# Kernel tuning notes

Hardware: AMD Instinct MI355X
Metric: run time of the kernel (lower is better)

The kernel has to match this reference:

```python
import jax, jax.numpy as jnp
import numpy as np

G = 4  # groupsize((1,1)) = 4 -> C4 rotations, exact rot90 path


def _lift_filter(w):
    # w: (O, I, k, k) -> (O*G, I, k, k); orbit of 90-degree filter rotations
    f = jnp.stack([jnp.rot90(w, r, axes=(-2, -1)) for r in range(G)], axis=1)
    O, _, I, k, _ = f.shape
    return f.reshape(O * G, I, k, k)


def _group_filter(w):
    # w: (O, I, G, k, k) -> (O*G, I*G, k, k)
    # rotatestack_n: spatial rot90 by r, then cyclic shift of the group axis by r
    fs = []
    for r in range(G):
        roty = jnp.rot90(w, r, axes=(-2, -1))
        roty = jnp.roll(roty, r, axis=-3)  # new[i] = roty[(G - r + i) % G]
        fs.append(roty)
    f = jnp.stack(fs, axis=1)  # (O, G, I, G, k, k)
    O, _, I, _, k, _ = f.shape
    return f.reshape(O * G, I * G, k, k)


def _conv(x, f, b, pad):
    y = jax.lax.conv_general_dilated(x, f, (1, 1), [(pad, pad), (pad, pad)],
                                     dimension_numbers=('NCHW', 'OIHW', 'NCHW'))
    # bias is stacked per group element: repeat each out-channel bias G times
    return y + jnp.repeat(b, G)[None, :, None, None]


def _pool(x):
    return jax.lax.reduce_window(x, -jnp.inf, jax.lax.max, (1, 1, 2, 2), (1, 1, 2, 2), 'VALID')


def setup_inputs():
    key = jax.random.key(0)
    ks = jax.random.split(key, 16)
    ch = [6, 12, 12, 24, 24, 16]   # [24,48,48,96,96,64] // G
    kern = [7, 5, 5, 5, 5, 5]
    d = {'x': jax.random.normal(ks[0], (64, 1, 96, 96), jnp.float32)}
    d['w0'] = jax.random.normal(ks[1], (ch[0], 1, kern[0], kern[0]), jnp.float32) / np.sqrt(ch[0] * 1.0)
    d['b0'] = jnp.zeros((ch[0],), jnp.float32)
    for i in range(1, 6):
        std = 1.0 / np.sqrt(float(ch[i] * ch[i - 1]))
        d['w%d' % i] = jax.random.normal(ks[1 + i], (ch[i], ch[i - 1], G, kern[i], kern[i]), jnp.float32) * std
        d['b%d' % i] = jnp.zeros((ch[i],), jnp.float32)
    d['fw1'] = jax.random.normal(ks[8], (64, 64), jnp.float32) * 0.05
    d['fb1'] = jnp.zeros((64,), jnp.float32)
    d['fw2'] = jax.random.normal(ks[9], (10, 64), jnp.float32) * 0.05
    d['fb2'] = jnp.zeros((10,), jnp.float32)
    return d


def reference(x, w0, b0, w1, b1, w2, b2, w3, b3, w4, b4, w5, b5, fw1, fb1, fw2, fb2):
    h = jax.nn.relu(_conv(x, _lift_filter(w0), b0, 1))                  # (B,24,92,92)
    h = jax.nn.relu(_conv(h, _group_filter(w1), b1, 2))
    h = _pool(h)                                                        # (B,48,46,46)
    h = jax.nn.relu(_conv(h, _group_filter(w2), b2, 2))
    h = jax.nn.relu(_conv(h, _group_filter(w3), b3, 2))
    h = _pool(h)                                                        # (B,96,23,23)
    h = jax.nn.relu(_conv(h, _group_filter(w4), b4, 2))
    h = jax.nn.relu(_conv(h, _group_filter(w5), b5, 1))                 # (B,64,21,21)
    h = h.mean(axis=(-2, -1))                                           # (B,64) flat (out_ch*G)
    h = jax.nn.relu(h @ fw1.T + fb1)
    return h @ fw2.T + fb2                                              # (B,10)
```

## Files before the change

### kernel.cpp

```cpp
#include <hip/hip_runtime.h>
#include <hip/hip_bf16.h>


typedef short s16x8 __attribute__((ext_vector_type(8)));
typedef __bf16 bf16x8 __attribute__((ext_vector_type(8)));
typedef float f32x4 __attribute__((ext_vector_type(4)));
typedef unsigned short u16;
typedef unsigned int u32;

__device__ __forceinline__ u16 f2bf(float f) {
    unsigned u = __float_as_uint(f);
    return (u16)((u + 0x7FFFu + ((u >> 16) & 1u)) >> 16);
}
__device__ __forceinline__ float bf2f(u16 h) {
    return __uint_as_float(((unsigned)h) << 16);
}

__device__ __forceinline__ void rot_src(int r, int K, int y, int x, int& sy, int& sx) {
    switch (r & 3) {
        case 0: sy = y;         sx = x;         break;
        case 1: sy = x;         sx = K - 1 - y; break;
        case 2: sy = K - 1 - y; sx = K - 1 - x; break;
        default: sy = K - 1 - x; sx = y;        break;
    }
}

__global__ void lift_w0T_kernel(const float* __restrict__ w, float* __restrict__ f) {
    const int K = 7, KK = 49, OC = 24;
    int idx = blockIdx.x * blockDim.x + threadIdx.x;
    if (idx >= KK * OC) return;
    int oc = idx % OC; int kk = idx / OC;
    int y = kk / K, x = kk % K;
    int r = oc & 3, o = oc >> 2;
    int sy, sx; rot_src(r, K, y, x, sy, sx);
    f[idx] = w[o * KK + sy * K + sx];
}

__global__ void wfrag_kernel(const float* __restrict__ w, u16* __restrict__ wf,
                             int O, int I, int KC, int NT, int total) {
    int idx = blockIdx.x * blockDim.x + threadIdx.x;
    if (idx >= total) return;
    int j = idx & 7;
    int lane = (idx >> 3) & 63;
    int rest = idx >> 9;
    int nc = rest % NT; rest /= NT;
    int kc = rest % KC; int kpos = rest / KC;
    int ky = kpos / 5, kx = kpos % 5;
    int kk = ((lane >> 4) << 3) + j;
    int ic = kc * 32 + kk;
    int oc = nc * 16 + (lane & 15);
    float val = 0.f;
    if (ic < I * 4) {
        int o = oc >> 2, r = oc & 3, i = ic >> 2, s = ic & 3;
        int g = (s - r + 4) & 3;
        int sy, sx; rot_src(r, 5, ky, kx, sy, sx);
        val = w[(((o * I + i) * 4 + g) * 25) + sy * 5 + sx];
    }
    u16 hb = f2bf(val);
    u16 lb = f2bf(val - bf2f(hb));
    wf[idx] = hb;
    wf[idx + total] = lb;
}

__global__ void pad_x_kernel(const float* __restrict__ x, float* __restrict__ xp) {
    int idx = blockIdx.x * blockDim.x + threadIdx.x;
    if (idx >= 64 * 96 * 96) return;
    int c = idx % 96; int t = idx / 96;
    int r = t % 96; int n = t / 96;
    xp[((size_t)n * 98 + r + 1) * 100 + c + 1] = x[idx];
}

__global__ void prep_halo_kernel(u16* __restrict__ buf, long LO, int NHW,
                                 int Hp, int Wp, int ICO) {
    int idx = blockIdx.x * blockDim.x + threadIdx.x;
    if (idx >= NHW) return;
    int c = idx % Wp; int t = idx / Wp;
    int r = t % Hp; int n = t / Hp;
    bool halo = (r < 2) || (r >= Hp - 2) || (c < 2) || (c >= Wp - 2);
    if (!halo) return;
    size_t base = (((size_t)n * Hp + r) * Wp + c) * ICO;
    s16x8 z = {0, 0, 0, 0, 0, 0, 0, 0};
    for (int cc = 0; cc < (ICO >> 3); ++cc) {
        *(s16x8*)(buf + base + cc * 8) = z;
        *(s16x8*)(buf + LO + base + cc * 8) = z;
    }
}

__global__ __launch_bounds__(256) void conv0_kernel(
        const float* __restrict__ xp, const float* __restrict__ f0t,
        const float* __restrict__ b0, u16* __restrict__ p1, long p1LO) {
    int idx = blockIdx.x * blockDim.x + threadIdx.x;
    if (idx >= 64 * 92 * 23) return;
    int xq = idx % 23; int t = idx / 23;
    int oy = t % 92; int n = t / 92;
    float acc[24][4];
#pragma unroll
    for (int a = 0; a < 24; ++a)
#pragma unroll
        for (int b = 0; b < 4; ++b) acc[a][b] = 0.f;

    const float* ip = xp + ((size_t)n * 98 + oy) * 100 + xq * 4;
#pragma unroll
    for (int ky = 0; ky < 7; ++ky) {
        const float* row = ip + (size_t)ky * 100;
        float xv[12];
#pragma unroll
        for (int v = 0; v < 3; ++v)
            *reinterpret_cast<float4*>(&xv[4 * v]) =
                *reinterpret_cast<const float4*>(row + 4 * v);
#pragma unroll
        for (int kx = 0; kx < 7; ++kx) {
            const float* wp = f0t + (ky * 7 + kx) * 24;
#pragma unroll
            for (int qd = 0; qd < 6; ++qd) {
                float4 wv = *reinterpret_cast<const float4*>(wp + qd * 4);
#pragma unroll
                for (int jx = 0; jx < 4; ++jx) {
                    acc[qd * 4 + 0][jx] = fmaf(wv.x, xv[kx + jx], acc[qd * 4 + 0][jx]);
                    acc[qd * 4 + 1][jx] = fmaf(wv.y, xv[kx + jx], acc[qd * 4 + 1][jx]);
                    acc[qd * 4 + 2][jx] = fmaf(wv.z, xv[kx + jx], acc[qd * 4 + 2][jx]);
                    acc[qd * 4 + 3][jx] = fmaf(wv.w, xv[kx + jx], acc[qd * 4 + 3][jx]);
                }
            }
        }
    }
    float bv[6];
#pragma unroll
    for (int qd = 0; qd < 6; ++qd) bv[qd] = b0[qd];

    size_t ob = (((size_t)n * 96 + oy + 2) * 96 + xq * 4 + 2) * 24;
#pragma unroll
    for (int jx = 0; jx < 4; ++jx) {
        s16x8 hv[3], lv[3];
#pragma unroll
        for (int cc = 0; cc < 3; ++cc)
#pragma unroll
            for (int e = 0; e < 8; ++e) {
                int ch = cc * 8 + e;
                float v = fmaxf(acc[ch][jx] + bv[ch >> 2], 0.f);
                u16 hb = f2bf(v);
                u16 lb = f2bf(v - bf2f(hb));
                hv[cc][e] = (short)hb; lv[cc][e] = (short)lb;
            }
#pragma unroll
        for (int cc = 0; cc < 3; ++cc) {
            *(s16x8*)(p1 + ob + jx * 24 + cc * 8) = hv[cc];
            *(s16x8*)(p1 + p1LO + ob + jx * 24 + cc * 8) = lv[cc];
        }
    }
}

template <int IC32, int ICIN, int NT, int NTW, int MT, int CR, int SW, bool POOL,
          int XOFF, int OCO, bool TRANS, int PMODE>
__global__ __launch_bounds__(SW*(NT/NTW)*64, 2) void conv_mfma_kernel(
        const u16* __restrict__ act, long actLO,
        const u16* __restrict__ wf, int wfLO,
        const float* __restrict__ bias,
        u16* __restrict__ outP, long outLO,
        float* __restrict__ outF,
        int Hp, int Wp, int OH, int OW, int PH, int POW,
        int NRG, int NXS, int HpO, int WpO) {
    constexpr int OG = NT / NTW;
    constexpr int NW = SW * OG;
    constexpr int KC = IC32 / 32;
    constexpr int WT = MT * 16 + 4 + XOFF;
    constexpr int R  = CR * SW + 4;
    constexpr int CHUNKS = R * WT * 8;
    constexpr int TROWS = POOL ? SW : CR * SW;
    constexpr int TX = POOL ? MT * 8 : MT * 16;
    constexpr int SX = OCO + 4;
    constexpr int STAGE_B = CHUNKS * 16;
    constexpr int TRAN_B = TRANS ? TROWS * TX * SX * 4 : 0;
    constexpr int LDSB = STAGE_B > TRAN_B ? STAGE_B : TRAN_B;
    __shared__ __align__(16) char ldsraw[LDSB];
    u16* lds = (u16*)ldsraw;

    int q8 = gridDim.x >> 3;
    int wid = (blockIdx.x & 7) * q8 + (blockIdx.x >> 3);
    int xs = wid % NXS; int t0 = wid / NXS;
    int rgrp = t0 % NRG; int n = t0 / NRG;

    int BR = rgrp * (CR * SW);
    int rbase = BR + XOFF;
    int xbase = xs * (MT * 16);

    int tid = threadIdx.x;
    int wv = tid >> 6;
    int lane = tid & 63;
    int l15 = lane & 15, lg = lane >> 4;
    int og = wv % OG, rg = wv / OG;

    f32x4 accP[CR][MT][NTW], accQ[CR][MT][NTW];
#pragma unroll
    for (int cr = 0; cr < CR; ++cr)
#pragma unroll
        for (int m = 0; m < MT; ++m)
#pragma unroll
            for (int nc = 0; nc < NTW; ++nc) {
                accP[cr][m][nc] = f32x4{0.f, 0.f, 0.f, 0.f};
                accQ[cr][m][nc] = f32x4{0.f, 0.f, 0.f, 0.f};
            }

    const u16* wfl = wf + (size_t)lane * 8;
    const u16* actn = act + ((size_t)n * Hp) * Wp * ICIN;

    for (int kcp = 0; kcp < KC; ++kcp) {
        if (kcp) __syncthreads();
        for (int u = tid; u < CHUNKS; u += NW * 64) {
            int c = u & 7; int rest = u >> 3;
            int xl = rest % WT; int row = rest / WT;
            int cg = c ^ (xl & 7);
            int sp = cg >> 2, cc4 = cg & 3;
            int gx = xbase + xl, gr = rbase + row;
            int ch0 = (kcp * 4 + cc4) * 8;
            s16x8 v = {0, 0, 0, 0, 0, 0, 0, 0};
            if (gx < Wp && gr < Hp && ch0 < ICIN)
                v = *(const s16x8*)(actn + (size_t)sp * actLO +
                      ((size_t)gr * Wp + gx) * ICIN + ch0);
            *(s16x8*)&lds[(size_t)u * 8] = v;
        }
        __syncthreads();

        auto loadB = [&](int w, bf16x8 (&bh)[NTW], bf16x8 (&bl)[NTW]) {
            const u16* bp = wfl + ((size_t)(w * KC + kcp) * NT + og * NTW) * 512;
#pragma unroll
            for (int nc = 0; nc < NTW; ++nc) {
                bh[nc] = *(const bf16x8*)(bp + nc * 512);
                bl[nc] = *(const bf16x8*)(bp + nc * 512 + wfLO);
            }
        };

        if constexpr (PMODE == 1) {
            auto loadA = [&](int w, bf16x8 (&ah)[MT][CR], bf16x8 (&al)[MT][CR]) {
                int wky = w / 5, wkx = w - wky * 5;
#pragma unroll
                for (int m = 0; m < MT; ++m) {
                    int xl = m * 16 + XOFF + l15 + wkx;
                    int sw = xl & 7;
#pragma unroll
                    for (int cr = 0; cr < CR; ++cr) {
                        int row = rg * CR + cr + wky;
                        int base = (row * WT + xl) * 8;
                        ah[m][cr] = *(const bf16x8*)&lds[(size_t)(base + (lg ^ sw)) * 8];
                        al[m][cr] = *(const bf16x8*)&lds[(size_t)(base + ((4 + lg) ^ sw)) * 8];
                    }
                }
            };
            auto mfmaBlk = [&](bf16x8 (&bh)[NTW], bf16x8 (&bl)[NTW],
                               bf16x8 (&ah)[MT][CR], bf16x8 (&al)[MT][CR]) {
#pragma unroll
                for (int m = 0; m < MT; ++m)
#pragma unroll
                    for (int nc = 0; nc < NTW; ++nc)
#pragma unroll
                        for (int cr = 0; cr < CR; ++cr) {
                            accP[cr][m][nc] = __builtin_amdgcn_mfma_f32_16x16x32_bf16(
                                ah[m][cr], bh[nc], accP[cr][m][nc], 0, 0, 0);
                            accQ[cr][m][nc] = __builtin_amdgcn_mfma_f32_16x16x32_bf16(
                                ah[m][cr], bl[nc], accQ[cr][m][nc], 0, 0, 0);
                            accQ[cr][m][nc] = __builtin_amdgcn_mfma_f32_16x16x32_bf16(
                                al[m][cr], bh[nc], accQ[cr][m][nc], 0, 0, 0);
                        }
            };
            bf16x8 bhX[NTW], blX[NTW], ahX[MT][CR], alX[MT][CR];
            bf16x8 bhY[NTW], blY[NTW], ahY[MT][CR], alY[MT][CR];
            loadB(0, bhX, blX); loadA(0, ahX, alX);
            for (int t = 0; t < 12; ++t) {
                loadB(2 * t + 1, bhY, blY); loadA(2 * t + 1, ahY, alY);
                mfmaBlk(bhX, blX, ahX, alX);
                loadB(2 * t + 2, bhX, blX); loadA(2 * t + 2, ahX, alX);
                mfmaBlk(bhY, blY, ahY, alY);
            }
            mfmaBlk(bhX, blX, ahX, alX);
        } else {
            auto window = [&](int w, bf16x8 (&bh)[NTW], bf16x8 (&bl)[NTW]) {
                int wky = w / 5, wkx = w - wky * 5;
#pragma unroll
                for (int m = 0; m < MT; ++m) {
                    int xl = m * 16 + XOFF + l15 + wkx;
                    int sw = xl & 7;
                    bf16x8 ah[CR], al[CR];
#pragma unroll
                    for (int cr = 0; cr < CR; ++cr) {
                        int row = rg * CR + cr + wky;
                        int base = (row * WT + xl) * 8;
                        ah[cr] = *(const bf16x8*)&lds[(size_t)(base + (lg ^ sw)) * 8];
                        al[cr] = *(const bf16x8*)&lds[(size_t)(base + ((4 + lg) ^ sw)) * 8];
                    }
#pragma unroll
                    for (int nc = 0; nc < NTW; ++nc)
#pragma unroll
                        for (int cr = 0; cr < CR; ++cr) {
                            accP[cr][m][nc] = __builtin_amdgcn_mfma_f32_16x16x32_bf16(
                                ah[cr], bh[nc], accP[cr][m][nc], 0, 0, 0);
                            accQ[cr][m][nc] = __builtin_amdgcn_mfma_f32_16x16x32_bf16(
                                ah[cr], bl[nc], accQ[cr][m][nc], 0, 0, 0);
                            accQ[cr][m][nc] = __builtin_amdgcn_mfma_f32_16x16x32_bf16(
                                al[cr], bh[nc], accQ[cr][m][nc], 0, 0, 0);
                        }
                }
            };
            bf16x8 bhX[NTW], blX[NTW], bhY[NTW], blY[NTW];
            loadB(0, bhX, blX);
            for (int t = 0; t < 12; ++t) {
                loadB(2 * t + 1, bhY, blY);
                window(2 * t, bhX, blX);
                loadB(2 * t + 2, bhX, blX);
                window(2 * t + 1, bhY, blY);
            }
            window(24, bhX, blX);
        }
    }

    if constexpr (TRANS) {
        __syncthreads();
        u32* ldsw = (u32*)ldsraw;
#pragma unroll
        for (int nc = 0; nc < NTW; ++nc) {
            int oc = (og * NTW + nc) * 16 + l15;
            float bv = bias[oc >> 2];
#pragma unroll
            for (int m = 0; m < MT; ++m) {
                if constexpr (POOL) {
                    float c0[4], c1[4];
#pragma unroll
                    for (int j = 0; j < 4; ++j) {
                        c0[j] = accP[0][m][nc][j] + accQ[0][m][nc][j];
                        c1[j] = accP[1][m][nc][j] + accQ[1][m][nc][j];
                    }
#pragma unroll
                    for (int a2 = 0; a2 < 2; ++a2) {
                        float mx = fmaxf(fmaxf(c0[2 * a2], c0[2 * a2 + 1]),
                                         fmaxf(c1[2 * a2], c1[2 * a2 + 1]));
                        float v = fmaxf(mx + bv, 0.f);
                        u16 hb = f2bf(v);
                        u16 lb = f2bf(v - bf2f(hb));
                        int px = m * 8 + lg * 2 + a2;
                        ldsw[(rg * TX + px) * SX + oc] = ((u32)hb << 16) | lb;
                    }
                } else {
#pragma unroll
                    for (int cr = 0; cr < CR; ++cr)
#pragma unroll
                        for (int j = 0; j < 4; ++j) {
                            float v = fmaxf(accP[cr][m][nc][j] + accQ[cr][m][nc][j] + bv, 0.f);
                            u16 hb = f2bf(v);
                            u16 lb = f2bf(v - bf2f(hb));
                            int xloc = m * 16 + lg * 4 + j;
                            ldsw[((rg * CR + cr) * TX + xloc) * SX + oc] =
                                ((u32)hb << 16) | lb;
                        }
                }
            }
        }
        __syncthreads();
        constexpr int CPX = OCO / 8;
        constexpr int TOT = TROWS * TX * 2 * CPX;
        int OHL = POOL ? PH : OH;
        int OWL = POOL ? POW : OW;
        int obr = POOL ? rgrp * SW : BR;
        int obx = POOL ? (xbase >> 1) : xbase;
        for (int u = tid; u < TOT; u += NW * 64) {
            int c = u % CPX; int rest = u / CPX;
            int pl = rest & 1; rest >>= 1;
            int x = rest % TX; int row = rest / TX;
            int gr = obr + row, gx = obx + x;
            if (gr >= OHL || gx >= OWL) continue;
            s16x8 v = {0, 0, 0, 0, 0, 0, 0, 0};
            if (c * 8 < NT * 16) {
                const u32* p = &ldsw[(row * TX + x) * SX + c * 8];
                uint4 w0 = *(const uint4*)p;
                uint4 w1 = *(const uint4*)(p + 4);
                if (pl == 0) {
                    v[0] = (short)(w0.x >> 16); v[1] = (short)(w0.y >> 16);
                    v[2] = (short)(w0.z >> 16); v[3] = (short)(w0.w >> 16);
                    v[4] = (short)(w1.x >> 16); v[5] = (short)(w1.y >> 16);
                    v[6] = (short)(w1.z >> 16); v[7] = (short)(w1.w >> 16);
                } else {
                    v[0] = (short)(w0.x & 0xffff); v[1] = (short)(w0.y & 0xffff);
                    v[2] = (short)(w0.z & 0xffff); v[3] = (short)(w0.w & 0xffff);
                    v[4] = (short)(w1.x & 0xffff); v[5] = (short)(w1.y & 0xffff);
                    v[6] = (short)(w1.z & 0xffff); v[7] = (short)(w1.w & 0xffff);
                }
            }
            *(s16x8*)(outP + (size_t)pl * outLO +
                      (((size_t)n * HpO + gr + 2) * WpO + gx + 2) * OCO + c * 8) = v;
        }
    } else {
#pragma unroll
        for (int nc = 0; nc < NTW; ++nc) {
            int oc = (og * NTW + nc) * 16 + l15;
            float bv = bias[oc >> 2];
#pragma unroll
            for (int m = 0; m < MT; ++m) {
                int gx0 = xbase + m * 16;
#pragma unroll
                for (int cr = 0; cr < CR; ++cr) {
                    int oy = BR + rg * CR + cr;
                    if (oy < OH) {
#pragma unroll
                        for (int j = 0; j < 4; ++j) {
                            int gx = gx0 + lg * 4 + j;
                            if (gx < OW) {
                                float v = fmaxf(accP[cr][m][nc][j] + accQ[cr][m][nc][j] + bv, 0.f);
                                outF[(((size_t)n * OH + oy) * OW + gx) * (NT * 16) + oc] = v;
                            }
                        }
                    }
                }
            }
        }
    }
}

__global__ void mean_nhwc_kernel(const float* __restrict__ in, float* __restrict__ out) {
    __shared__ float sm[256];
    int n = blockIdx.x;
    int c = threadIdx.x & 63, q = threadIdx.x >> 6;
    float s = 0.f;
    for (int p = q; p < 441; p += 4) s += in[((size_t)n * 441 + p) * 64 + c];
    sm[threadIdx.x] = s;
    __syncthreads();
    if (q == 0) out[n * 64 + c] = (sm[c] + sm[c + 64] + sm[c + 128] + sm[c + 192]) * (1.0f / 441.0f);
}

__global__ void fc_kernel(const float* __restrict__ mean, const float* __restrict__ fw1,
                          const float* __restrict__ fb1, const float* __restrict__ fw2,
                          const float* __restrict__ fb2, float* __restrict__ out) {
    __shared__ float m[4096];
    __shared__ float h1[4096];
    int tid = threadIdx.x;
    for (int i = tid; i < 4096; i += 256) m[i] = mean[i];
    __syncthreads();
    for (int i = tid; i < 4096; i += 256) {
        int n = i >> 6, j = i & 63;
        float s = fb1[j];
        for (int k = 0; k < 64; ++k) s = fmaf(m[n * 64 + k], fw1[j * 64 + k], s);
        h1[i] = fmaxf(s, 0.f);
    }
    __syncthreads();
    for (int i = tid; i < 640; i += 256) {
        int n = i / 10, j2 = i % 10;
        float s = fb2[j2];
        for (int j = 0; j < 64; ++j) s = fmaf(h1[n * 64 + j], fw2[j2 * 64 + j], s);
        out[i] = s;
    }
}

extern "C" void kernel_launch(void* const* d_in, const int* in_sizes, int n_in,
                              void* d_out, int out_size, void* d_ws, size_t ws_size,
                              hipStream_t stream) {
    const float* x   = (const float*)d_in[0];
    const float* w0  = (const float*)d_in[1];
    const float* b0  = (const float*)d_in[2];
    const float* w1  = (const float*)d_in[3];
    const float* b1  = (const float*)d_in[4];
    const float* w2  = (const float*)d_in[5];
    const float* b2  = (const float*)d_in[6];
    const float* w3  = (const float*)d_in[7];
    const float* b3  = (const float*)d_in[8];
    const float* w4  = (const float*)d_in[9];
    const float* b4  = (const float*)d_in[10];
    const float* w5  = (const float*)d_in[11];
    const float* b5  = (const float*)d_in[12];
    const float* fw1 = (const float*)d_in[13];
    const float* fb1 = (const float*)d_in[14];
    const float* fw2 = (const float*)d_in[15];
    const float* fb2 = (const float*)d_in[16];

    char* ws = (char*)d_ws;
    if (ws_size < 128827392ull) return;

    float* F0   = (float*)(ws + 0);
    u16*   WF1  = (u16*)(ws + 8192);
    u16*   WF2  = (u16*)(ws + 161792);
    u16*   WF3  = (u16*)(ws + 468992);
    u16*   WF4  = (u16*)(ws + 1083392);
    u16*   WF5  = (u16*)(ws + 2004992);
    float* MEANB= (float*)(ws + 2619392);
    float* XP   = (float*)(ws + 2635776);
    float* C5   = (float*)(ws + 5144576);
    u16*   A    = (u16*)(ws + 12369920);
    u16*   B    = (u16*)(ws + 87867392);
    const long P1LO = 14155776;
    const long P2LO = 10240000;
    const long P4LO = 4478976;

    hipLaunchKernelGGL(lift_w0T_kernel, dim3(5), dim3(256), 0, stream, w0, F0);
    hipLaunchKernelGGL(wfrag_kernel, dim3(150), dim3(256), 0, stream, w1, WF1, 12, 6, 1, 3, 38400);
    hipLaunchKernelGGL(wfrag_kernel, dim3(300), dim3(256), 0, stream, w2, WF2, 12, 12, 2, 3, 76800);
    hipLaunchKernelGGL(wfrag_kernel, dim3(600), dim3(256), 0, stream, w3, WF3, 24, 12, 2, 6, 153600);
    hipLaunchKernelGGL(wfrag_kernel, dim3(900), dim3(256), 0, stream, w4, WF4, 24, 24, 3, 6, 230400);
    hipLaunchKernelGGL(wfrag_kernel, dim3(600), dim3(256), 0, stream, w5, WF5, 16, 24, 3, 4, 153600);

    hipMemsetAsync(XP, 0, 2508800, stream);
    hipLaunchKernelGGL(pad_x_kernel, dim3(2304), dim3(256), 0, stream, x, XP);

    hipLaunchKernelGGL(prep_halo_kernel, dim3(2304), dim3(256), 0, stream,
                       A, P1LO, 64*96*96, 96, 96, 24);
    hipLaunchKernelGGL(conv0_kernel, dim3((64*92*23 + 255)/256), dim3(256), 0, stream,
                       XP, F0, b0, A, P1LO);

    hipLaunchKernelGGL(prep_halo_kernel, dim3(625), dim3(256), 0, stream,
                       B, P2LO, 64*50*50, 50, 50, 64);
    hipLaunchKernelGGL((conv_mfma_kernel<32, 24, 3, 3, 3, 2, 4, true, 0, 64, true, 0>),
                       dim3(1536), dim3(256), 0, stream,
                       A, P1LO, WF1, 38400, b1, B, P2LO, (float*)nullptr,
                       96, 96, 92, 92, 46, 46, 12, 2, 50, 50);

    hipLaunchKernelGGL(prep_halo_kernel, dim3(625), dim3(256), 0, stream,
                       A, P2LO, 64*50*50, 50, 50, 64);
    hipLaunchKernelGGL((conv_mfma_kernel<64, 64, 3, 3, 3, 1, 4, false, 0, 64, true, 1>),
                       dim3(768), dim3(256), 0, stream,
                       B, P2LO, WF2, 76800, b2, A, P2LO, (float*)nullptr,
                       50, 50, 46, 46, 0, 0, 12, 1, 50, 50);

    hipLaunchKernelGGL(prep_halo_kernel, dim3(183), dim3(256), 0, stream,
                       B, P4LO, 64*27*27, 27, 27, 96);
    hipLaunchKernelGGL((conv_mfma_kernel<64, 64, 6, 3, 3, 2, 2, true, 0, 96, true, 0>),
                       dim3(768), dim3(256), 0, stream,
                       A, P2LO, WF3, 153600, b3, B, P4LO, (float*)nullptr,
                       50, 50, 46, 46, 23, 23, 12, 1, 27, 27);

    hipLaunchKernelGGL(prep_halo_kernel, dim3(183), dim3(256), 0, stream,
                       A, P4LO, 64*27*27, 27, 27, 96);
    hipLaunchKernelGGL((conv_mfma_kernel<96, 96, 6, 3, 2, 2, 2, false, 0, 96, true, 1>),
                       dim3(384), dim3(256), 0, stream,
                       B, P4LO, WF4, 230400, b4, A, P4LO, (float*)nullptr,
                       27, 27, 23, 23, 0, 0, 6, 1, 27, 27);

    hipLaunchKernelGGL((conv_mfma_kernel<96, 96, 4, 2, 2, 2, 2, false, 1, 96, false, 1>),
                       dim3(384), dim3(256), 0, stream,
                       A, P4LO, WF5, 153600, b5, (u16*)A, 0, C5,
                       27, 27, 21, 21, 0, 0, 6, 1, 27, 27);

    hipLaunchKernelGGL(mean_nhwc_kernel, dim3(64), dim3(256), 0, stream, C5, MEANB);
    hipLaunchKernelGGL(fc_kernel, dim3(1), dim3(256), 0, stream,
                       MEANB, fw1, fb1, fw2, fb2, (float*)d_out);
}
```

Measured before the change: 571.8 us.

## Fold kx taps into K dimension for layer-1 conv to cut padded MFMA work

Layer 1 has only 24 input channels, so the old kernel padded each 32-wide K chunk per tap and wasted a quarter of the MFMA work. The new conv_fold_kernel packs (kx, channel-octet) pairs into K chunks of 32, giving 20 steps instead of 25. A new weight-fragment kernel lays weights out to match. The step loop is fully unrolled with double-buffered B loads, which adds register pressure and irregular LDS indexing per lane group.

```diff
diff --git a/kernel.cpp b/kernel.cpp
--- a/kernel.cpp
+++ b/kernel.cpp
@@ -62,6 +62,34 @@
     wf[idx + total] = lb;
 }
 
+__global__ void wfrag_fold_kernel(const float* __restrict__ w, u16* __restrict__ wf,
+                                  int O, int I, int PASSES, int NT, int ICR8,
+                                  int total) {
+    int idx = blockIdx.x * blockDim.x + threadIdx.x;
+    if (idx >= total) return;
+    int j = idx & 7;
+    int lane = (idx >> 3) & 63;
+    int rest = idx >> 9;
+    int nc = rest % NT; rest /= NT;
+    int p = rest % PASSES; int ky = rest / PASSES;
+    int kchunk = p * 4 + (lane >> 4);
+    float val = 0.f;
+    if (kchunk < 5 * ICR8) {
+        int kx = kchunk / ICR8;
+        int icc = kchunk - kx * ICR8;
+        int ic = icc * 8 + j;
+        int oc = nc * 16 + (lane & 15);
+        int o = oc >> 2, r = oc & 3, i = ic >> 2, s = ic & 3;
+        int g = (s - r + 4) & 3;
+        int sy, sx; rot_src(r, 5, ky, kx, sy, sx);
+        val = w[(((o * I + i) * 4 + g) * 25) + sy * 5 + sx];
+    }
+    u16 hb = f2bf(val);
+    u16 lb = f2bf(val - bf2f(hb));
+    wf[idx] = hb;
+    wf[idx + total] = lb;
+}
+
 __global__ void pad_x_kernel(const float* __restrict__ x, float* __restrict__ xp) {
     int idx = blockIdx.x * blockDim.x + threadIdx.x;
     if (idx >= 64 * 96 * 96) return;
@@ -150,9 +178,9 @@
     }
 }
 
-template <int IC32, int ICIN, int NT, int NTW, int MT, int CR, int SW, bool POOL,
-          int XOFF, int OCO, bool TRANS, int PMODE>
-__global__ __launch_bounds__(SW*(NT/NTW)*64, 2) void conv_mfma_kernel(
+template <int ICR8, int ICIN, int PASSES, int NT, int NTW, int MT, int CR, int SW,
+          bool POOL, int XOFF, int OCO, bool TRANS>
+__global__ __launch_bounds__(SW*(NT/NTW)*64, 2) void conv_fold_kernel(
         const u16* __restrict__ act, long actLO,
         const u16* __restrict__ wf, int wfLO,
         const float* __restrict__ bias,
@@ -162,7 +190,6 @@
         int NRG, int NXS, int HpO, int WpO) {
     constexpr int OG = NT / NTW;
     constexpr int NW = SW * OG;
-    constexpr int KC = IC32 / 32;
     constexpr int WT = MT * 16 + 4 + XOFF;
     constexpr int R  = CR * SW + 4;
     constexpr int CHUNKS = R * WT * 8;
@@ -204,111 +231,64 @@
     const u16* wfl = wf + (size_t)lane * 8;
     const u16* actn = act + ((size_t)n * Hp) * Wp * ICIN;
 
-    for (int kcp = 0; kcp < KC; ++kcp) {
-        if (kcp) __syncthreads();
-        for (int u = tid; u < CHUNKS; u += NW * 64) {
-            int c = u & 7; int rest = u >> 3;
-            int xl = rest % WT; int row = rest / WT;
-            int cg = c ^ (xl & 7);
-            int sp = cg >> 2, cc4 = cg & 3;
-            int gx = xbase + xl, gr = rbase + row;
-            int ch0 = (kcp * 4 + cc4) * 8;
-            s16x8 v = {0, 0, 0, 0, 0, 0, 0, 0};
-            if (gx < Wp && gr < Hp && ch0 < ICIN)
-                v = *(const s16x8*)(actn + (size_t)sp * actLO +
-                      ((size_t)gr * Wp + gx) * ICIN + ch0);
-            *(s16x8*)&lds[(size_t)u * 8] = v;
-        }
-        __syncthreads();
-
-        auto loadB = [&](int w, bf16x8 (&bh)[NTW], bf16x8 (&bl)[NTW]) {
-            const u16* bp = wfl + ((size_t)(w * KC + kcp) * NT + og * NTW) * 512;
-#pragma unroll
-            for (int nc = 0; nc < NTW; ++nc) {
-                bh[nc] = *(const bf16x8*)(bp + nc * 512);
-                bl[nc] = *(const bf16x8*)(bp + nc * 512 + wfLO);
-            }
-        };
-
-        if constexpr (PMODE == 1) {
-            auto loadA = [&](int w, bf16x8 (&ah)[MT][CR], bf16x8 (&al)[MT][CR]) {
-                int wky = w / 5, wkx = w - wky * 5;
-#pragma unroll
-                for (int m = 0; m < MT; ++m) {
-                    int xl = m * 16 + XOFF + l15 + wkx;
-                    int sw = xl & 7;
-#pragma unroll
-                    for (int cr = 0; cr < CR; ++cr) {
-                        int row = rg * CR + cr + wky;
-                        int base = (row * WT + xl) * 8;
-                        ah[m][cr] = *(const bf16x8*)&lds[(size_t)(base + (lg ^ sw)) * 8];
-                        al[m][cr] = *(const bf16x8*)&lds[(size_t)(base + ((4 + lg) ^ sw)) * 8];
-                    }
-                }
-            };
-            auto mfmaBlk = [&](bf16x8 (&bh)[NTW], bf16x8 (&bl)[NTW],
-                               bf16x8 (&ah)[MT][CR], bf16x8 (&al)[MT][CR]) {
-#pragma unroll
-                for (int m = 0; m < MT; ++m)
-#pragma unroll
-                    for (int nc = 0; nc < NTW; ++nc)
-#pragma unroll
-                        for (int cr = 0; cr < CR; ++cr) {
-                            accP[cr][m][nc] = __builtin_amdgcn_mfma_f32_16x16x32_bf16(
-                                ah[m][cr], bh[nc], accP[cr][m][nc], 0, 0, 0);
-                            accQ[cr][m][nc] = __builtin_amdgcn_mfma_f32_16x16x32_bf16(
-                                ah[m][cr], bl[nc], accQ[cr][m][nc], 0, 0, 0);
-                            accQ[cr][m][nc] = __builtin_amdgcn_mfma_f32_16x16x32_bf16(
-                                al[m][cr], bh[nc], accQ[cr][m][nc], 0, 0, 0);
-                        }
-            };
-            bf16x8 bhX[NTW], blX[NTW], ahX[MT][CR], alX[MT][CR];
-            bf16x8 bhY[NTW], blY[NTW], ahY[MT][CR], alY[MT][CR];
-            loadB(0, bhX, blX); loadA(0, ahX, alX);
-            for (int t = 0; t < 12; ++t) {
-                loadB(2 * t + 1, bhY, blY); loadA(2 * t + 1, ahY, alY);
-                mfmaBlk(bhX, blX, ahX, alX);
-                loadB(2 * t + 2, bhX, blX); loadA(2 * t + 2, ahX, alX);
-                mfmaBlk(bhY, blY, ahY, alY);
-            }
-            mfmaBlk(bhX, blX, ahX, alX);
-        } else {
-            auto window = [&](int w, bf16x8 (&bh)[NTW], bf16x8 (&bl)[NTW]) {
-                int wky = w / 5, wkx = w - wky * 5;
-#pragma unroll
-                for (int m = 0; m < MT; ++m) {
-                    int xl = m * 16 + XOFF + l15 + wkx;
-                    int sw = xl & 7;
-                    bf16x8 ah[CR], al[CR];
-#pragma unroll
-                    for (int cr = 0; cr < CR; ++cr) {
-                        int row = rg * CR + cr + wky;
-                        int base = (row * WT + xl) * 8;
-                        ah[cr] = *(const bf16x8*)&lds[(size_t)(base + (lg ^ sw)) * 8];
-                        al[cr] = *(const bf16x8*)&lds[(size_t)(base + ((4 + lg) ^ sw)) * 8];
-                    }
-#pragma unroll
-                    for (int nc = 0; nc < NTW; ++nc)
-#pragma unroll
-                        for (int cr = 0; cr < CR; ++cr) {
-                            accP[cr][m][nc] = __builtin_amdgcn_mfma_f32_16x16x32_bf16(
-                                ah[cr], bh[nc], accP[cr][m][nc], 0, 0, 0);
-                            accQ[cr][m][nc] = __builtin_amdgcn_mfma_f32_16x16x32_bf16(
-                                ah[cr], bl[nc], accQ[cr][m][nc], 0, 0, 0);
-                            accQ[cr][m][nc] = __builtin_amdgcn_mfma_f32_16x16x32_bf16(
-                                al[cr], bh[nc], accQ[cr][m][nc], 0, 0, 0);
-                        }
-                }
-            };
-            bf16x8 bhX[NTW], blX[NTW], bhY[NTW], blY[NTW];
-            loadB(0, bhX, blX);
-            for (int t = 0; t < 12; ++t) {
-                loadB(2 * t + 1, bhY, blY);
-                window(2 * t, bhX, blX);
-                loadB(2 * t + 2, bhX, blX);
-                window(2 * t + 1, bhY, blY);
-            }
-            window(24, bhX, blX);
+    for (int u = tid; u < CHUNKS; u += NW * 64) {
+        int c = u & 7; int rest = u >> 3;
+        int xl = rest % WT; int row = rest / WT;
+        int cg = c ^ (xl & 7);
+        int gx = xbase + xl, gr = rbase + row;
+        s16x8 v = {0, 0, 0, 0, 0, 0, 0, 0};
+        if (cg < 2 * ICR8 && gx < Wp && gr < Hp) {
+            int sp = cg < ICR8 ? 0 : 1;
+            int icc = cg < ICR8 ? cg : cg - ICR8;
+            v = *(const s16x8*)(actn + (size_t)sp * actLO +
+                  ((size_t)gr * Wp + gx) * ICIN + icc * 8);
+        }
+        *(s16x8*)&lds[(size_t)u * 8] = v;
+    }
+    __syncthreads();
+
+    constexpr int STEPS = 5 * PASSES;
+    auto loadBf = [&](int s, bf16x8 (&bh)[NTW], bf16x8 (&bl)[NTW]) {
+        const u16* bp = wfl + ((size_t)s * NT + og * NTW) * 512;
+#pragma unroll
+        for (int nc = 0; nc < NTW; ++nc) {
+            bh[nc] = *(const bf16x8*)(bp + nc * 512);
+            bl[nc] = *(const bf16x8*)(bp + nc * 512 + wfLO);
+        }
+    };
+    bf16x8 bhD[2][NTW], blD[2][NTW];
+    loadBf(0, bhD[0], blD[0]);
+#pragma unroll
+    for (int s = 0; s < STEPS; ++s) {
+        if (s + 1 < STEPS) loadBf(s + 1, bhD[(s + 1) & 1], blD[(s + 1) & 1]);
+        const int ky = s / PASSES, p = s % PASSES;
+        int kc2 = p * 4 + lg;
+        int kx = kc2 / ICR8;
+        int icc = kc2 - kx * ICR8;
+        if (kx > 4) { kx = 4; icc = 0; }
+#pragma unroll
+        for (int m = 0; m < MT; ++m) {
+            int xl = m * 16 + XOFF + l15 + kx;
+            int sw = xl & 7;
+            bf16x8 ah[CR], al[CR];
+#pragma unroll
+            for (int cr = 0; cr < CR; ++cr) {
+                int row = rg * CR + cr + ky;
+                int base = (row * WT + xl) * 8;
+                ah[cr] = *(const bf16x8*)&lds[(size_t)(base + (icc ^ sw)) * 8];
+                al[cr] = *(const bf16x8*)&lds[(size_t)(base + ((ICR8 + icc) ^ sw)) * 8];
+            }
+#pragma unroll
+            for (int nc = 0; nc < NTW; ++nc)
+#pragma unroll
+                for (int cr = 0; cr < CR; ++cr) {
+                    accP[cr][m][nc] = __builtin_amdgcn_mfma_f32_16x16x32_bf16(
+                        ah[cr], bhD[s & 1][nc], accP[cr][m][nc], 0, 0, 0);
+                    accQ[cr][m][nc] = __builtin_amdgcn_mfma_f32_16x16x32_bf16(
+                        ah[cr], blD[s & 1][nc], accQ[cr][m][nc], 0, 0, 0);
+                    accQ[cr][m][nc] = __builtin_amdgcn_mfma_f32_16x16x32_bf16(
+                        al[cr], bhD[s & 1][nc], accQ[cr][m][nc], 0, 0, 0);
+                }
         }
     }
 
@@ -413,6 +393,269 @@
     }
 }
 
+template <int IC32, int ICIN, int NT, int NTW, int MT, int CR, int SW, bool POOL,
+          int XOFF, int OCO, bool TRANS, int PMODE>
+__global__ __launch_bounds__(SW*(NT/NTW)*64, 2) void conv_mfma_kernel(
+        const u16* __restrict__ act, long actLO,
+        const u16* __restrict__ wf, int wfLO,
+        const float* __restrict__ bias,
+        u16* __restrict__ outP, long outLO,
+        float* __restrict__ outF,
+        int Hp, int Wp, int OH, int OW, int PH, int POW,
+        int NRG, int NXS, int HpO, int WpO) {
+    constexpr int OG = NT / NTW;
+    constexpr int NW = SW * OG;
+    constexpr int KC = IC32 / 32;
+    constexpr int WT = MT * 16 + 4 + XOFF;
+    constexpr int R  = CR * SW + 4;
+    constexpr int CHUNKS = R * WT * 8;
+    constexpr int TROWS = POOL ? SW : CR * SW;
+    constexpr int TX = POOL ? MT * 8 : MT * 16;
+    constexpr int SX = OCO + 4;
+    constexpr int STAGE_B = CHUNKS * 16;
+    constexpr int TRAN_B = TRANS ? TROWS * TX * SX * 4 : 0;
+    constexpr int LDSB = STAGE_B > TRAN_B ? STAGE_B : TRAN_B;
+    __shared__ __align__(16) char ldsraw[LDSB];
+    u16* lds = (u16*)ldsraw;
+
+    int q8 = gridDim.x >> 3;
+    int wid = (blockIdx.x & 7) * q8 + (blockIdx.x >> 3);
+    int xs = wid % NXS; int t0 = wid / NXS;
+    int rgrp = t0 % NRG; int n = t0 / NRG;
+
+    int BR = rgrp * (CR * SW);
+    int rbase = BR + XOFF;
+    int xbase = xs * (MT * 16);
+
+    int tid = threadIdx.x;
+    int wv = tid >> 6;
+    int lane = tid & 63;
+    int l15 = lane & 15, lg = lane >> 4;
+    int og = wv % OG, rg = wv / OG;
+
+    f32x4 accP[CR][MT][NTW], accQ[CR][MT][NTW];
+#pragma unroll
+    for (int cr = 0; cr < CR; ++cr)
+#pragma unroll
+        for (int m = 0; m < MT; ++m)
+#pragma unroll
+            for (int nc = 0; nc < NTW; ++nc) {
+                accP[cr][m][nc] = f32x4{0.f, 0.f, 0.f, 0.f};
+                accQ[cr][m][nc] = f32x4{0.f, 0.f, 0.f, 0.f};
+            }
+
+    const u16* wfl = wf + (size_t)lane * 8;
+    const u16* actn = act + ((size_t)n * Hp) * Wp * ICIN;
+
+    for (int kcp = 0; kcp < KC; ++kcp) {
+        if (kcp) __syncthreads();
+        for (int u = tid; u < CHUNKS; u += NW * 64) {
+            int c = u & 7; int rest = u >> 3;
+            int xl = rest % WT; int row = rest / WT;
+            int cg = c ^ (xl & 7);
+            int sp = cg >> 2, cc4 = cg & 3;
+            int gx = xbase + xl, gr = rbase + row;
+            int ch0 = (kcp * 4 + cc4) * 8;
+            s16x8 v = {0, 0, 0, 0, 0, 0, 0, 0};
+            if (gx < Wp && gr < Hp && ch0 < ICIN)
+                v = *(const s16x8*)(actn + (size_t)sp * actLO +
+                      ((size_t)gr * Wp + gx) * ICIN + ch0);
+            *(s16x8*)&lds[(size_t)u * 8] = v;
+        }
+        __syncthreads();
+
+        auto loadB = [&](int w, bf16x8 (&bh)[NTW], bf16x8 (&bl)[NTW]) {
+            const u16* bp = wfl + ((size_t)(w * KC + kcp) * NT + og * NTW) * 512;
+#pragma unroll
+            for (int nc = 0; nc < NTW; ++nc) {
+                bh[nc] = *(const bf16x8*)(bp + nc * 512);
+                bl[nc] = *(const bf16x8*)(bp + nc * 512 + wfLO);
+            }
+        };
+
+        if constexpr (PMODE == 1) {
+            auto loadA = [&](int w, bf16x8 (&ah)[MT][CR], bf16x8 (&al)[MT][CR]) {
+                int wky = w / 5, wkx = w - wky * 5;
+#pragma unroll
+                for (int m = 0; m < MT; ++m) {
+                    int xl = m * 16 + XOFF + l15 + wkx;
+                    int sw = xl & 7;
+#pragma unroll
+                    for (int cr = 0; cr < CR; ++cr) {
+                        int row = rg * CR + cr + wky;
+                        int base = (row * WT + xl) * 8;
+                        ah[m][cr] = *(const bf16x8*)&lds[(size_t)(base + (lg ^ sw)) * 8];
+                        al[m][cr] = *(const bf16x8*)&lds[(size_t)(base + ((4 + lg) ^ sw)) * 8];
+                    }
+                }
+            };
+            auto mfmaBlk = [&](bf16x8 (&bh)[NTW], bf16x8 (&bl)[NTW],
+                               bf16x8 (&ah)[MT][CR], bf16x8 (&al)[MT][CR]) {
+#pragma unroll
+                for (int m = 0; m < MT; ++m)
+#pragma unroll
+                    for (int nc = 0; nc < NTW; ++nc)
+#pragma unroll
+                        for (int cr = 0; cr < CR; ++cr) {
+                            accP[cr][m][nc] = __builtin_amdgcn_mfma_f32_16x16x32_bf16(
+                                ah[m][cr], bh[nc], accP[cr][m][nc], 0, 0, 0);
+                            accQ[cr][m][nc] = __builtin_amdgcn_mfma_f32_16x16x32_bf16(
+                                ah[m][cr], bl[nc], accQ[cr][m][nc], 0, 0, 0);
+                            accQ[cr][m][nc] = __builtin_amdgcn_mfma_f32_16x16x32_bf16(
+                                al[m][cr], bh[nc], accQ[cr][m][nc], 0, 0, 0);
+                        }
+            };
+            bf16x8 bhX[NTW], blX[NTW], ahX[MT][CR], alX[MT][CR];
+            bf16x8 bhY[NTW], blY[NTW], ahY[MT][CR], alY[MT][CR];
+            loadB(0, bhX, blX); loadA(0, ahX, alX);
+            for (int t = 0; t < 12; ++t) {
+                loadB(2 * t + 1, bhY, blY); loadA(2 * t + 1, ahY, alY);
+                mfmaBlk(bhX, blX, ahX, alX);
+                loadB(2 * t + 2, bhX, blX); loadA(2 * t + 2, ahX, alX);
+                mfmaBlk(bhY, blY, ahY, alY);
+            }
+            mfmaBlk(bhX, blX, ahX, alX);
+        } else {
+            auto window = [&](int w, bf16x8 (&bh)[NTW], bf16x8 (&bl)[NTW]) {
+                int wky = w / 5, wkx = w - wky * 5;
+#pragma unroll
+                for (int m = 0; m < MT; ++m) {
+                    int xl = m * 16 + XOFF + l15 + wkx;
+                    int sw = xl & 7;
+                    bf16x8 ah[CR], al[CR];
+#pragma unroll
+                    for (int cr = 0; cr < CR; ++cr) {
+                        int row = rg * CR + cr + wky;
+                        int base = (row * WT + xl) * 8;
+                        ah[cr] = *(const bf16x8*)&lds[(size_t)(base + (lg ^ sw)) * 8];
+                        al[cr] = *(const bf16x8*)&lds[(size_t)(base + ((4 + lg) ^ sw)) * 8];
+                    }
+#pragma unroll
+                    for (int nc = 0; nc < NTW; ++nc)
+#pragma unroll
+                        for (int cr = 0; cr < CR; ++cr) {
+                            accP[cr][m][nc] = __builtin_amdgcn_mfma_f32_16x16x32_bf16(
+                                ah[cr], bh[nc], accP[cr][m][nc], 0, 0, 0);
+                            accQ[cr][m][nc] = __builtin_amdgcn_mfma_f32_16x16x32_bf16(
+                                ah[cr], bl[nc], accQ[cr][m][nc], 0, 0, 0);
+                            accQ[cr][m][nc] = __builtin_amdgcn_mfma_f32_16x16x32_bf16(
+                                al[cr], bh[nc], accQ[cr][m][nc], 0, 0, 0);
+                        }
+                }
+            };
+            bf16x8 bhX[NTW], blX[NTW], bhY[NTW], blY[NTW];
+            loadB(0, bhX, blX);
+            for (int t = 0; t < 12; ++t) {
+                loadB(2 * t + 1, bhY, blY);
+                window(2 * t, bhX, blX);
+                loadB(2 * t + 2, bhX, blX);
+                window(2 * t + 1, bhY, blY);
+            }
+            window(24, bhX, blX);
+        }
+    }
+
+    if constexpr (TRANS) {
+        __syncthreads();
+        u32* ldsw = (u32*)ldsraw;
+#pragma unroll
+        for (int nc = 0; nc < NTW; ++nc) {
+            int oc = (og * NTW + nc) * 16 + l15;
+            float bv = bias[oc >> 2];
+#pragma unroll
+            for (int m = 0; m < MT; ++m) {
+                if constexpr (POOL) {
+                    float c0[4], c1[4];
+#pragma unroll
+                    for (int j = 0; j < 4; ++j) {
+                        c0[j] = accP[0][m][nc][j] + accQ[0][m][nc][j];
+                        c1[j] = accP[1][m][nc][j] + accQ[1][m][nc][j];
+                    }
+#pragma unroll
+                    for (int a2 = 0; a2 < 2; ++a2) {
+                        float mx = fmaxf(fmaxf(c0[2 * a2], c0[2 * a2 + 1]),
+                                         fmaxf(c1[2 * a2], c1[2 * a2 + 1]));
+                        float v = fmaxf(mx + bv, 0.f);
+                        u16 hb = f2bf(v);
+                        u16 lb = f2bf(v - bf2f(hb));
+                        int px = m * 8 + lg * 2 + a2;
+                        ldsw[(rg * TX + px) * SX + oc] = ((u32)hb << 16) | lb;
+                    }
+                } else {
+#pragma unroll
+                    for (int cr = 0; cr < CR; ++cr)
+#pragma unroll
+                        for (int j = 0; j < 4; ++j) {
+                            float v = fmaxf(accP[cr][m][nc][j] + accQ[cr][m][nc][j] + bv, 0.f);
+                            u16 hb = f2bf(v);
+                            u16 lb = f2bf(v - bf2f(hb));
+                            int xloc = m * 16 + lg * 4 + j;
+                            ldsw[((rg * CR + cr) * TX + xloc) * SX + oc] =
+                                ((u32)hb << 16) | lb;
+                        }
+                }
+            }
+        }
+        __syncthreads();
+        constexpr int CPX = OCO / 8;
+        constexpr int TOT = TROWS * TX * 2 * CPX;
+        int OHL = POOL ? PH : OH;
+        int OWL = POOL ? POW : OW;
+        int obr = POOL ? rgrp * SW : BR;
+        int obx = POOL ? (xbase >> 1) : xbase;
+        for (int u = tid; u < TOT; u += NW * 64) {
+            int c = u % CPX; int rest = u / CPX;
+            int pl = rest & 1; rest >>= 1;
+            int x = rest % TX; int row = rest / TX;
+            int gr = obr + row, gx = obx + x;
+            if (gr >= OHL || gx >= OWL) continue;
+            s16x8 v = {0, 0, 0, 0, 0, 0, 0, 0};
+            if (c * 8 < NT * 16) {
+                const u32* p = &ldsw[(row * TX + x) * SX + c * 8];
+                uint4 w0 = *(const uint4*)p;
+                uint4 w1 = *(const uint4*)(p + 4);
+                if (pl == 0) {
+                    v[0] = (short)(w0.x >> 16); v[1] = (short)(w0.y >> 16);
+                    v[2] = (short)(w0.z >> 16); v[3] = (short)(w0.w >> 16);
+                    v[4] = (short)(w1.x >> 16); v[5] = (short)(w1.y >> 16);
+                    v[6] = (short)(w1.z >> 16); v[7] = (short)(w1.w >> 16);
+                } else {
+                    v[0] = (short)(w0.x & 0xffff); v[1] = (short)(w0.y & 0xffff);
+                    v[2] = (short)(w0.z & 0xffff); v[3] = (short)(w0.w & 0xffff);
+                    v[4] = (short)(w1.x & 0xffff); v[5] = (short)(w1.y & 0xffff);
+                    v[6] = (short)(w1.z & 0xffff); v[7] = (short)(w1.w & 0xffff);
+                }
+            }
+            *(s16x8*)(outP + (size_t)pl * outLO +
+                      (((size_t)n * HpO + gr + 2) * WpO + gx + 2) * OCO + c * 8) = v;
+        }
+    } else {
+#pragma unroll
+        for (int nc = 0; nc < NTW; ++nc) {
+            int oc = (og * NTW + nc) * 16 + l15;
+            float bv = bias[oc >> 2];
+#pragma unroll
+            for (int m = 0; m < MT; ++m) {
+                int gx0 = xbase + m * 16;
+#pragma unroll
+                for (int cr = 0; cr < CR; ++cr) {
+                    int oy = BR + rg * CR + cr;
+                    if (oy < OH) {
+#pragma unroll
+                        for (int j = 0; j < 4; ++j) {
+                            int gx = gx0 + lg * 4 + j;
+                            if (gx < OW) {
+                                float v = fmaxf(accP[cr][m][nc][j] + accQ[cr][m][nc][j] + bv, 0.f);
+                                outF[(((size_t)n * OH + oy) * OW + gx) * (NT * 16) + oc] = v;
+                            }
+                        }
+                    }
+                }
+            }
+        }
+    }
+}
+
 __global__ void mean_nhwc_kernel(const float* __restrict__ in, float* __restrict__ out) {
     __shared__ float sm[256];
     int n = blockIdx.x;
@@ -487,7 +730,8 @@
     const long P4LO = 4478976;
 
     hipLaunchKernelGGL(lift_w0T_kernel, dim3(5), dim3(256), 0, stream, w0, F0);
-    hipLaunchKernelGGL(wfrag_kernel, dim3(150), dim3(256), 0, stream, w1, WF1, 12, 6, 1, 3, 38400);
+    hipLaunchKernelGGL(wfrag_fold_kernel, dim3(120), dim3(256), 0, stream,
+                       w1, WF1, 12, 6, 4, 3, 3, 30720);
     hipLaunchKernelGGL(wfrag_kernel, dim3(300), dim3(256), 0, stream, w2, WF2, 12, 12, 2, 3, 76800);
     hipLaunchKernelGGL(wfrag_kernel, dim3(600), dim3(256), 0, stream, w3, WF3, 24, 12, 2, 6, 153600);
     hipLaunchKernelGGL(wfrag_kernel, dim3(900), dim3(256), 0, stream, w4, WF4, 24, 24, 3, 6, 230400);
@@ -503,9 +747,9 @@
 
     hipLaunchKernelGGL(prep_halo_kernel, dim3(625), dim3(256), 0, stream,
                        B, P2LO, 64*50*50, 50, 50, 64);
-    hipLaunchKernelGGL((conv_mfma_kernel<32, 24, 3, 3, 3, 2, 4, true, 0, 64, true, 0>),
+    hipLaunchKernelGGL((conv_fold_kernel<3, 24, 4, 3, 3, 3, 2, 4, true, 0, 64, true>),
                        dim3(1536), dim3(256), 0, stream,
-                       A, P1LO, WF1, 38400, b1, B, P2LO, (float*)nullptr,
+                       A, P1LO, WF1, 30720, b1, B, P2LO, (float*)nullptr,
                        96, 96, 92, 92, 46, 46, 12, 2, 50, 50);
 
     hipLaunchKernelGGL(prep_halo_kernel, dim3(625), dim3(256), 0, stream,
```

New measurement: 728.1 us. +27.3%, slower.
